# Optimization experiments

Hardware: AMD Instinct MI355X
Metric: run time of the kernel (lower is better)

Reference implementation:

```python
import jax, jax.numpy as jnp
import numpy as np
import math

EMBED_DIM = 128
NUM_HEADS = 16
HEAD_DIM = EMBED_DIM // NUM_HEADS  # = 8 = n_wires of the quantum circuit


def setup_inputs() -> dict:
    key = jax.random.key(0)
    k1, k2, k3 = jax.random.split(key, 3)
    B, S = 4, 2048
    x = jax.random.normal(k1, (B, S, EMBED_DIM), dtype=jnp.float32)
    # shared trainable RX angles of the single q_layer (applied to every head)
    theta = jax.random.normal(k2, (HEAD_DIM,), dtype=jnp.float32)
    w_out = jax.random.normal(k3, (EMBED_DIM, EMBED_DIM), dtype=jnp.float32) / math.sqrt(EMBED_DIM)
    mask = jnp.ones((B, S), dtype=jnp.int32)
    return {"x": x, "theta": theta, "w_out": w_out, "mask": mask}


def quantum_linear(x_head, theta):
    # Circuit: RX(x_i) encode + RX(theta_i) on wire i, CNOT chain (i, i+1),
    # then <Z_j>. For product state |psi_i> = RX(phi_i)|0>, <Z_i> = cos(phi_i),
    # and the CNOT chain gives final <Z_j> = prod_{i<=j} cos(phi_i).
    phi = x_head + theta  # [..., D] broadcast over leading dims
    return jnp.cumprod(jnp.cos(phi), axis=-1)


def reference(x, theta, w_out, mask):
    B, S, E = x.shape
    H, D = NUM_HEADS, HEAD_DIM
    xs = x.reshape(B, S, H, D)
    q = quantum_linear(xs, theta).transpose(0, 2, 1, 3)  # [B, H, S, D]; k = v = q
    scores = jnp.einsum("bhsd,bhtd->bhst", q, q) / math.sqrt(D)
    scores = jnp.where(mask[:, None, None, :] == 0, -1e9, scores)
    probs = jax.nn.softmax(scores, axis=-1)  # dropout is identity in eval
    attn = jnp.einsum("bhst,bhtd->bhsd", probs, q)
    attn = attn.transpose(0, 2, 1, 3).reshape(B, S, E)
    return attn @ w_out.T
```

## Files before the change

### kernel.cpp

```cpp
#include <hip/hip_runtime.h>
#include <hip/hip_bf16.h>
#include <hip/hip_fp16.h>

#define NB 4
#define NS 2048
#define NE 128
#define NH 16
#define ND 8

#define VT_BLK 144
#define VT_BH (128 * VT_BLK)

typedef __attribute__((ext_vector_type(8))) _Float16 half8;
typedef __attribute__((ext_vector_type(4))) float f32x4;
typedef __attribute__((ext_vector_type(16))) float f32x16;

__device__ __forceinline__ unsigned int pkrtz(float a, float b) {
    typedef __fp16 fp16v2 __attribute__((ext_vector_type(2)));
    union { fp16v2 h; unsigned int u; } v;
    v.h = __builtin_amdgcn_cvt_pkrtz(a, b);
    return v.u;
}
__device__ __forceinline__ unsigned short f2h(float a) {
    return __half_as_ushort(__float2half(a));
}
__device__ __forceinline__ half8 mk_half8(unsigned u0, unsigned u1,
                                          unsigned u2, unsigned u3) {
    union { half8 h; unsigned u[4]; } v;
    v.u[0] = u0; v.u[1] = u1; v.u[2] = u2; v.u[3] = u3;
    return v.h;
}

__device__ __forceinline__ void qrow(const float* __restrict__ xp,
                                     const float* th, float* p) {
    float4 a = *(const float4*)xp, c = *(const float4*)(xp + 4);
    float t = 1.f;
    t *= cosf(a.x + th[0]); p[0] = t;
    t *= cosf(a.y + th[1]); p[1] = t;
    t *= cosf(a.z + th[2]); p[2] = t;
    t *= cosf(a.w + th[3]); p[3] = t;
    t *= cosf(c.x + th[4]); p[4] = t;
    t *= cosf(c.y + th[5]); p[5] = t;
    t *= cosf(c.z + th[6]); p[6] = t;
    t *= cosf(c.w + th[7]); p[7] = t;
}

__global__ __launch_bounds__(256) void qgen_kernel(
        const float* __restrict__ x,
        const float* __restrict__ theta,
        const int* __restrict__ mask,
        const float* __restrict__ w,
        unsigned short* __restrict__ qg,
        unsigned short* __restrict__ vtg,
        unsigned short* __restrict__ wf16) {
    const int gid = blockIdx.x * 256 + threadIdx.x;
    const int bh = gid >> 10;
    const int b = bh >> 4, h = bh & (NH - 1);
    const int j = gid & 1023;
    const int s0 = 2 * j;
    const float SC = 0.71421629f;

    if (blockIdx.x == 0) {
        for (int i = threadIdx.x; i < 2048; i += 256) {
            const float* wp = w + i * 8;
            float4 a = *(const float4*)wp, c = *(const float4*)(wp + 4);
            uint4 pk;
            pk.x = pkrtz(a.x, a.y); pk.y = pkrtz(a.z, a.w);
            pk.z = pkrtz(c.x, c.y); pk.w = pkrtz(c.z, c.w);
            *(uint4*)&wf16[i * 8] = pk;
        }
    }

    float th[ND];
#pragma unroll
    for (int d = 0; d < ND; d++) th[d] = theta[d];

    float p0[ND], p1[ND];
    qrow(x + ((size_t)(b * NS + s0) * NE + h * ND), th, p0);
    qrow(x + ((size_t)(b * NS + s0 + 1) * NE + h * ND), th, p1);
    const float mz0 = mask[b * NS + s0] ? 1.f : 0.f;
    const float mz1 = mask[b * NS + s0 + 1] ? 1.f : 0.f;

    uint4 qa, qb;
    qa.x = pkrtz(p0[0] * SC, p0[1] * SC);
    qa.y = pkrtz(p0[2] * SC, p0[3] * SC);
    qa.z = pkrtz(p0[4] * SC, p0[5] * SC);
    qa.w = pkrtz(p0[6] * SC, p0[7] * SC);
    qb.x = pkrtz(p1[0] * SC, p1[1] * SC);
    qb.y = pkrtz(p1[2] * SC, p1[3] * SC);
    qb.z = pkrtz(p1[4] * SC, p1[5] * SC);
    qb.w = pkrtz(p1[6] * SC, p1[7] * SC);
    *(uint4*)&qg[((size_t)bh * NS + s0) * ND] = qa;
    *(uint4*)&qg[((size_t)bh * NS + s0 + 1) * ND] = qb;

    const int blk = s0 >> 4, u = s0 & 15;
    const int k2 = (u & 3) | (((u >> 3) & 1) << 2) | (((u >> 2) & 1) << 3);
    unsigned short* vb = vtg + (size_t)bh * VT_BH + blk * VT_BLK + k2;
#pragma unroll
    for (int d = 0; d < ND; d++)
        *(unsigned int*)&vb[d * 16] = pkrtz(p0[d] * mz0, p1[d] * mz1);
    *(unsigned int*)&vb[8 * 16] = pkrtz(mz0, mz1);
}

__global__ __launch_bounds__(256) void attn_kernel(
        const unsigned short* __restrict__ qg,
        const unsigned short* __restrict__ vtg,
        unsigned short* __restrict__ mid) {
    const int bid = blockIdx.x;
    const int bh = bid >> 4;
    const int b = bh >> 4, h = bh & (NH - 1);
    const int msix = bid & 15;
    const int tid = threadIdx.x;

    const int wave = tid >> 6, lane = tid & 63;
    const int l31 = lane & 31, hi = lane >> 5;
    const int mb = msix * 128 + wave * 32;

    half8 hz = {0, 0, 0, 0, 0, 0, 0, 0};
    half8 bm = hi ? hz : *(const half8*)&qg[((size_t)bh * NS + mb + l31) * ND];

    const unsigned short* qt = qg + (size_t)bh * NS * ND + (size_t)l31 * ND;
    const int dv = (l31 < 9) ? l31 : 8;
    const unsigned short* vb = vtg + (size_t)bh * VT_BH + dv * 16 + hi * 8;

    f32x16 O = {0.f};
    const f32x16 zc = {0.f};

    for (int ch = 0; ch < 64; ch++) {
        half8 at = *(const half8*)&qt[(size_t)ch * 32 * ND];
        half8 vf1 = *(const half8*)&vb[ch * 2 * VT_BLK];
        half8 vf2 = *(const half8*)&vb[ch * 2 * VT_BLK + VT_BLK];

        f32x16 s = __builtin_amdgcn_mfma_f32_32x32x16_f16(at, bm, zc, 0, 0, 0);

        half8 pA1 = mk_half8(
            pkrtz(__builtin_amdgcn_exp2f(s[0]),  __builtin_amdgcn_exp2f(s[1])),
            pkrtz(__builtin_amdgcn_exp2f(s[2]),  __builtin_amdgcn_exp2f(s[3])),
            pkrtz(__builtin_amdgcn_exp2f(s[4]),  __builtin_amdgcn_exp2f(s[5])),
            pkrtz(__builtin_amdgcn_exp2f(s[6]),  __builtin_amdgcn_exp2f(s[7])));
        half8 pA2 = mk_half8(
            pkrtz(__builtin_amdgcn_exp2f(s[8]),  __builtin_amdgcn_exp2f(s[9])),
            pkrtz(__builtin_amdgcn_exp2f(s[10]), __builtin_amdgcn_exp2f(s[11])),
            pkrtz(__builtin_amdgcn_exp2f(s[12]), __builtin_amdgcn_exp2f(s[13])),
            pkrtz(__builtin_amdgcn_exp2f(s[14]), __builtin_amdgcn_exp2f(s[15])));

        O = __builtin_amdgcn_mfma_f32_32x32x16_f16(pA1, vf1, O, 0, 0, 0);
        O = __builtin_amdgcn_mfma_f32_32x32x16_f16(pA2, vf2, O, 0, 0, 0);
    }

#pragma unroll
    for (int r = 0; r < 16; r++) {
        float lsum = __shfl(O[r], (lane & 32) | 8, 64);
        float v = O[r] / lsum;
        if (l31 < ND) {
            int m = mb + (r & 3) + 8 * (r >> 2) + 4 * hi;
            mid[(size_t)(b * NS + m) * NE + h * ND + l31] = f2h(v);
        }
    }
}

__global__ __launch_bounds__(512) void proj_kernel(
        const unsigned short* __restrict__ mid,
        const unsigned short* __restrict__ wf16,
        float* __restrict__ out) {
    const int rb = blockIdx.x * 16;
    const int tid = threadIdx.x;
    const int wavei = tid >> 6, lane = tid & 63;
    const int quad = lane >> 4, l15 = lane & 15;
    const int n0 = wavei * 16;

    f32x4 acc = {0.f, 0.f, 0.f, 0.f};
#pragma unroll
    for (int kt = 0; kt < 4; kt++) {
        half8 af = *(const half8*)&mid[(size_t)(rb + l15) * NE + kt * 32 + quad * 8];
        half8 bf = *(const half8*)&wf16[(n0 + l15) * NE + kt * 32 + quad * 8];
        acc = __builtin_amdgcn_mfma_f32_16x16x32_f16(af, bf, acc, 0, 0, 0);
    }
#pragma unroll
    for (int r = 0; r < 4; r++)
        out[(size_t)(rb + quad * 4 + r) * NE + n0 + l15] = acc[r];
}

extern "C" void kernel_launch(void* const* d_in, const int* in_sizes, int n_in,
                              void* d_out, int out_size, void* d_ws, size_t ws_size,
                              hipStream_t stream) {
    const float* x     = (const float*)d_in[0];
    const float* theta = (const float*)d_in[1];
    const float* w_out = (const float*)d_in[2];
    const int*   mask  = (const int*)d_in[3];
    float* out = (float*)d_out;

    unsigned short* mid16 = (unsigned short*)d_ws;
    unsigned short* qg   = mid16 + (size_t)NB * NS * NE;
    unsigned short* vtg  = qg + (size_t)NB * NH * NS * ND;
    unsigned short* wf16 = vtg + (size_t)NB * NH * VT_BH;

    qgen_kernel<<<NB * NH * NS / 2 / 256, 256, 0, stream>>>(x, theta, mask, w_out,
                                                            qg, vtg, wf16);
    attn_kernel<<<NB * NH * 16, 256, 0, stream>>>(qg, vtg, mid16);
    proj_kernel<<<NB * NS / 16, 512, 0, stream>>>(mid16, wf16, out);
}
```

Baseline: 110.1 us.

## Split attention key range across two blocks and merge partials in projection

Each attention block now processes half of the key sequence, doubling the grid from 1024 to 2048 blocks. Unnormalized fp32 partial outputs and softmax denominators are written to workspace. The projection kernel sums the two halves, normalizes by the reciprocal of the combined denominator, converts to fp16 and feeds the MFMA. This is a split-K style change meant to raise occupancy and parallelism on a GPU with many CUs. The cost is extra fp32 intermediate traffic and more work in the projection kernel.

Measured after the change: 120.0 us. 9.0% more time.

```diff
diff --git a/kernel.cpp b/kernel.cpp
--- a/kernel.cpp
+++ b/kernel.cpp
@@ -20,9 +20,6 @@
     union { fp16v2 h; unsigned int u; } v;
     v.h = __builtin_amdgcn_cvt_pkrtz(a, b);
     return v.u;
-}
-__device__ __forceinline__ unsigned short f2h(float a) {
-    return __half_as_ushort(__float2half(a));
 }
 __device__ __forceinline__ half8 mk_half8(unsigned u0, unsigned u1,
                                           unsigned u2, unsigned u3) {
@@ -105,11 +102,13 @@
 __global__ __launch_bounds__(256) void attn_kernel(
         const unsigned short* __restrict__ qg,
         const unsigned short* __restrict__ vtg,
-        unsigned short* __restrict__ mid) {
+        float* __restrict__ mid32,
+        float* __restrict__ den) {
     const int bid = blockIdx.x;
-    const int bh = bid >> 4;
+    const int half = bid & 1;
+    const int msix = (bid >> 1) & 15;
+    const int bh = bid >> 5;
     const int b = bh >> 4, h = bh & (NH - 1);
-    const int msix = bid & 15;
     const int tid = threadIdx.x;
 
     const int wave = tid >> 6, lane = tid & 63;
@@ -119,14 +118,15 @@
     half8 hz = {0, 0, 0, 0, 0, 0, 0, 0};
     half8 bm = hi ? hz : *(const half8*)&qg[((size_t)bh * NS + mb + l31) * ND];
 
-    const unsigned short* qt = qg + (size_t)bh * NS * ND + (size_t)l31 * ND;
+    const unsigned short* qt = qg + ((size_t)bh * NS + half * 1024 + l31) * ND;
     const int dv = (l31 < 9) ? l31 : 8;
-    const unsigned short* vb = vtg + (size_t)bh * VT_BH + dv * 16 + hi * 8;
+    const unsigned short* vb = vtg + (size_t)bh * VT_BH + half * 64 * VT_BLK
+                             + dv * 16 + hi * 8;
 
     f32x16 O = {0.f};
     const f32x16 zc = {0.f};
 
-    for (int ch = 0; ch < 64; ch++) {
+    for (int ch = 0; ch < 32; ch++) {
         half8 at = *(const half8*)&qt[(size_t)ch * 32 * ND];
         half8 vf1 = *(const half8*)&vb[ch * 2 * VT_BLK];
         half8 vf2 = *(const half8*)&vb[ch * 2 * VT_BLK + VT_BLK];
@@ -148,19 +148,21 @@
         O = __builtin_amdgcn_mfma_f32_32x32x16_f16(pA2, vf2, O, 0, 0, 0);
     }
 
+    float* mp = mid32 + (size_t)half * NB * NS * NE;
+    float* dp = den + (size_t)half * NB * NS * NH;
 #pragma unroll
     for (int r = 0; r < 16; r++) {
-        float lsum = __shfl(O[r], (lane & 32) | 8, 64);
-        float v = O[r] / lsum;
-        if (l31 < ND) {
-            int m = mb + (r & 3) + 8 * (r >> 2) + 4 * hi;
-            mid[(size_t)(b * NS + m) * NE + h * ND + l31] = f2h(v);
-        }
+        int m = mb + (r & 3) + 8 * (r >> 2) + 4 * hi;
+        if (l31 < ND)
+            mp[(size_t)(b * NS + m) * NE + h * ND + l31] = O[r];
+        else if (l31 == ND)
+            dp[(size_t)(b * NS + m) * NH + h] = O[r];
     }
 }
 
 __global__ __launch_bounds__(512) void proj_kernel(
-        const unsigned short* __restrict__ mid,
+        const float* __restrict__ mid32,
+        const float* __restrict__ den,
         const unsigned short* __restrict__ wf16,
         float* __restrict__ out) {
     const int rb = blockIdx.x * 16;
@@ -169,11 +171,25 @@
     const int quad = lane >> 4, l15 = lane & 15;
     const int n0 = wavei * 16;
 
+    const size_t row = (size_t)(rb + l15);
+    const float* pa = mid32 + row * NE;
+    const float* pb = pa + (size_t)NB * NS * NE;
+    const float* da = den + row * NH;
+    const float* db = da + (size_t)NB * NS * NH;
+
     f32x4 acc = {0.f, 0.f, 0.f, 0.f};
 #pragma unroll
     for (int kt = 0; kt < 4; kt++) {
-        half8 af = *(const half8*)&mid[(size_t)(rb + l15) * NE + kt * 32 + quad * 8];
-        half8 bf = *(const half8*)&wf16[(n0 + l15) * NE + kt * 32 + quad * 8];
+        const int k0 = kt * 32 + quad * 8;
+        float4 a0 = *(const float4*)(pa + k0), a1 = *(const float4*)(pa + k0 + 4);
+        float4 b0 = *(const float4*)(pb + k0), b1 = *(const float4*)(pb + k0 + 4);
+        float rd = __builtin_amdgcn_rcpf(da[kt * 4 + quad] + db[kt * 4 + quad]);
+        half8 af = mk_half8(
+            pkrtz((a0.x + b0.x) * rd, (a0.y + b0.y) * rd),
+            pkrtz((a0.z + b0.z) * rd, (a0.w + b0.w) * rd),
+            pkrtz((a1.x + b1.x) * rd, (a1.y + b1.y) * rd),
+            pkrtz((a1.z + b1.z) * rd, (a1.w + b1.w) * rd));
+        half8 bf = *(const half8*)&wf16[(n0 + l15) * NE + k0];
         acc = __builtin_amdgcn_mfma_f32_16x16x32_f16(af, bf, acc, 0, 0, 0);
     }
 #pragma unroll
@@ -190,13 +206,14 @@
     const int*   mask  = (const int*)d_in[3];
     float* out = (float*)d_out;
 
-    unsigned short* mid16 = (unsigned short*)d_ws;
-    unsigned short* qg   = mid16 + (size_t)NB * NS * NE;
+    float* mid32 = (float*)d_ws;
+    float* den   = mid32 + (size_t)2 * NB * NS * NE;
+    unsigned short* qg   = (unsigned short*)(den + (size_t)2 * NB * NS * NH);
     unsigned short* vtg  = qg + (size_t)NB * NH * NS * ND;
     unsigned short* wf16 = vtg + (size_t)NB * NH * VT_BH;
 
     qgen_kernel<<<NB * NH * NS / 2 / 256, 256, 0, stream>>>(x, theta, mask, w_out,
                                                             qg, vtg, wf16);
-    attn_kernel<<<NB * NH * 16, 256, 0, stream>>>(qg, vtg, mid16);
-    proj_kernel<<<NB * NS / 16, 512, 0, stream>>>(mid16, wf16, out);
-}
+    attn_kernel<<<NB * NH * 16 * 2, 256, 0, stream>>>(qg, vtg, mid32, den);
+    proj_kernel<<<NB * NS / 16, 512, 0, stream>>>(mid32, den, wf16, out);
+}
```
